# Performance work log

Measured on AMD Instinct MI355X. Metric: run time of the kernel, lower is better.

## Reference

```python
import jax, jax.numpy as jnp
import numpy as np

N_HEADS = 16


def _apply_rope(x, cos, sin):
    # x: (B, T, H, hd); cos/sin: (max_len, hd//2)
    B, T, H, hd = x.shape
    c = cos[:T][None, :, None, :]  # (1, T, 1, hd//2)
    s = sin[:T][None, :, None, :]
    x1 = x[..., 0::2]
    x2 = x[..., 1::2]
    y1 = x1 * c - x2 * s
    y2 = x1 * s + x2 * c
    return jnp.stack((y1, y2), axis=-1).reshape(B, T, H, hd)


def _precompute_rope(head_dim, max_len):
    theta = 10000.0
    inv = 1.0 / theta ** (np.arange(0, head_dim, 2, dtype=np.float32) / head_dim)
    t = np.arange(max_len, dtype=np.float32)
    freqs = np.outer(t, inv)
    return jnp.asarray(np.cos(freqs)), jnp.asarray(np.sin(freqs))


def setup_inputs() -> dict:
    key = jax.random.key(0)
    k1, k2, k3 = jax.random.split(key, 3)
    B, T, C = 4, 2048, 2048
    hd = C // N_HEADS
    x = jax.random.normal(k1, (B, T, C), dtype=jnp.float32)
    w_attn = jax.random.normal(k2, (C, 3 * C), dtype=jnp.float32) * (C ** -0.5)
    w_proj = jax.random.normal(k3, (C, C), dtype=jnp.float32) * (C ** -0.5)
    rope_cos, rope_sin = _precompute_rope(hd, T)
    return {"x": x, "w_attn": w_attn, "w_proj": w_proj,
            "rope_cos": rope_cos, "rope_sin": rope_sin}


def reference(x, w_attn, w_proj, rope_cos, rope_sin):
    B, T, C = x.shape
    H = N_HEADS
    hd = C // H
    qkv = x @ w_attn  # (B, T, 3C)
    q, k, v = jnp.split(qkv, 3, axis=2)
    q = q.reshape(B, T, H, hd)
    k = k.reshape(B, T, H, hd)
    v = v.reshape(B, T, H, hd)
    q = _apply_rope(q, rope_cos, rope_sin)
    k = _apply_rope(k, rope_cos, rope_sin)
    scale = 1.0 / jnp.sqrt(jnp.asarray(hd, dtype=x.dtype))
    scores = jnp.einsum('bqhd,bkhd->bhqk', q, k) * scale  # (B, H, T, T)
    causal = jnp.tril(jnp.ones((T, T), dtype=bool))
    scores = jnp.where(causal[None, None], scores, jnp.finfo(scores.dtype).min)
    attn = jax.nn.softmax(scores, axis=-1)
    y = jnp.einsum('bhqk,bkhd->bqhd', attn, v).reshape(B, T, C)
    return y @ w_proj
```

## Files before the change

### kernel.cpp

```cpp
#include <hip/hip_runtime.h>
#include <cstdint>
#include <cstddef>

#define DEVI __device__ __forceinline__

typedef __attribute__((ext_vector_type(8))) short bf16x8;
typedef __attribute__((ext_vector_type(4))) float f32x4;

DEVI unsigned short f2bf(float f) {
  unsigned int u = __float_as_uint(f);
  u += 0x7fffu + ((u >> 16) & 1u);
  return (unsigned short)(u >> 16);
}
DEVI float bf2f(unsigned int us) { return __uint_as_float(us << 16); }

DEVI void gld_lds16(const void* g, void* l) {
  __builtin_amdgcn_global_load_lds(
      (const __attribute__((address_space(1))) void*)g,
      (__attribute__((address_space(3))) void*)l, 16, 0, 0);
}

__global__ __launch_bounds__(256) void k_conv(const float* __restrict__ in,
                                              short* __restrict__ out, int n4) {
  int i = blockIdx.x * 256 + threadIdx.x;
  if (i >= n4) return;
  float4 v = reinterpret_cast<const float4*>(in)[i];
  uint2 o;
  o.x = (unsigned)f2bf(v.x) | ((unsigned)f2bf(v.y) << 16);
  o.y = (unsigned)f2bf(v.z) | ((unsigned)f2bf(v.w) << 16);
  reinterpret_cast<uint2*>(out)[i] = o;
}

__global__ __launch_bounds__(256) void k_transpose(const float* __restrict__ in,
                                                   short* __restrict__ out,
                                                   int R, int Cc) {
  __shared__ short tile[64][66];
  int tcols = Cc >> 6;
  int tb = blockIdx.x % tcols;
  int rb = blockIdx.x / tcols;
  int tid = threadIdx.x;
#pragma unroll
  for (int rep = 0; rep < 16; ++rep) {
    int idx = rep * 256 + tid;
    int r = idx >> 6, c = idx & 63;
    tile[r][c] = (short)f2bf(in[(size_t)(rb * 64 + r) * Cc + tb * 64 + c]);
  }
  __syncthreads();
#pragma unroll
  for (int rep = 0; rep < 16; ++rep) {
    int idx = rep * 256 + tid;
    int r = idx >> 6, c = idx & 63;
    out[(size_t)(tb * 64 + r) * R + rb * 64 + c] = tile[c][r];
  }
}

template <int MODE, typename OutT>
__global__ __launch_bounds__(512, 2) void k_gemm8(const short* __restrict__ A,
                                                  const short* __restrict__ BT,
                                                  OutT* __restrict__ C,
                                                  int M, int N, int K,
                                                  const float* __restrict__ cosb,
                                                  const float* __restrict__ sinb,
                                                  short* __restrict__ Qr,
                                                  short* __restrict__ Kr,
                                                  short* __restrict__ VT) {
  __shared__ short sA[4][8192];
  __shared__ short sB[4][8192];
  const int tid = threadIdx.x;
  const int wv = tid >> 6, lane = tid & 63;
  const int l16 = lane & 15, lhi = lane >> 4;
  const int wr = wv >> 2, wc = wv & 3;
  const int bm = blockIdx.x * 256, bn = blockIdx.y * 256;
  const int srow0 = wv * 16 + (lane >> 2);
  const int sgs = lane & 3;
  const int NT = K >> 5;

  auto stageA = [&](int kt, int b) {
#pragma unroll
    for (int j = 0; j < 2; ++j) {
      int row = j * 128 + srow0;
      int g = sgs ^ ((row >> 1) & 3);
      gld_lds16(A + (size_t)(bm + row) * K + kt + g * 8,
                &sA[b][j * 4096 + wv * 512]);
    }
  };
  auto stageB = [&](int kt, int b) {
#pragma unroll
    for (int j = 0; j < 2; ++j) {
      int row = j * 128 + srow0;
      int g = sgs ^ ((row >> 1) & 3);
      gld_lds16(BT + (size_t)(bn + row) * K + kt + g * 8,
                &sB[b][j * 4096 + wv * 512]);
    }
  };

  f32x4 acc[8][4] = {};
  bf16x8 aP[8], bP[4], aQ[8], bQ[4];

#define FRAG_READ(DA, DB, BUF)                                                 \
  {                                                                            \
    const short* bufA_ = sA[(BUF)];                                            \
    const short* bufB_ = sB[(BUF)];                                            \
    _Pragma("unroll") for (int n = 0; n < 4; ++n) {                            \
      int row = wc * 64 + n * 16 + l16;                                        \
      DB[n] = *(const bf16x8*)&bufB_[row * 32 + ((lhi ^ ((row >> 1) & 3)) << 3)]; \
    }                                                                          \
    _Pragma("unroll") for (int m = 0; m < 8; ++m) {                            \
      int row = wr * 128 + m * 16 + l16;                                       \
      DA[m] = *(const bf16x8*)&bufA_[row * 32 + ((lhi ^ ((row >> 1) & 3)) << 3)]; \
    }                                                                          \
  }

#define TILE_BODY(T, CA, CB, NA, NB)                                           \
  {                                                                            \
    const int t_ = (T);                                                        \
    if (t_ + 1 < NT) FRAG_READ(NA, NB, (t_ + 1) & 3);                          \
    if (t_ + 3 < NT) {                                                         \
      stageA((t_ + 3) * 32, (t_ + 3) & 3);                                     \
      stageB((t_ + 3) * 32, (t_ + 3) & 3);                                     \
    }                                                                          \
    __builtin_amdgcn_sched_barrier(0);                                         \
    if (t_ + 3 < NT) {                                                         \
      asm volatile("s_waitcnt vmcnt(4)" ::: "memory");                         \
    } else {                                                                   \
      asm volatile("s_waitcnt vmcnt(0)" ::: "memory");                         \
    }                                                                          \
    __builtin_amdgcn_sched_barrier(0);                                         \
    __builtin_amdgcn_s_setprio(1);                                             \
    _Pragma("unroll") for (int m = 0; m < 8; ++m)                              \
        _Pragma("unroll") for (int n = 0; n < 4; ++n)                          \
            acc[m][n] = __builtin_amdgcn_mfma_f32_16x16x32_bf16(               \
                CA[m], CB[n], acc[m][n], 0, 0, 0);                             \
    __builtin_amdgcn_s_setprio(0);                                             \
    __builtin_amdgcn_sched_barrier(0);                                         \
    __builtin_amdgcn_s_barrier();                                              \
    __builtin_amdgcn_sched_barrier(0);                                         \
  }

  stageA(0, 0); stageB(0, 0);
  stageA(32, 1); stageB(32, 1);
  stageA(64, 2); stageB(64, 2);
  asm volatile("s_waitcnt vmcnt(8)" ::: "memory");
  __builtin_amdgcn_s_barrier();
  FRAG_READ(aP, bP, 0);
  asm volatile("s_waitcnt vmcnt(4)" ::: "memory");
  __builtin_amdgcn_s_barrier();
  __builtin_amdgcn_sched_barrier(0);

  for (int t = 0; t < NT; t += 2) {
    TILE_BODY(t, aP, bP, aQ, bQ);
    TILE_BODY(t + 1, aQ, bQ, aP, bP);
  }
#undef FRAG_READ
#undef TILE_BODY

  if constexpr (MODE == 1) {
#pragma unroll
    for (int m = 0; m < 8; ++m) {
#pragma unroll
      for (int n = 0; n < 4; ++n) {
        int col = bn + wc * 64 + n * 16 + l16;
#pragma unroll
        for (int r = 0; r < 4; ++r) {
          int row = bm + wr * 128 + m * 16 + lhi * 4 + r;
          C[(size_t)row * N + col] = acc[m][n][r];
        }
      }
    }
  } else {
    const int part = bn >> 11;
    const float kC = 0.08838834764831845f * 1.44269504088896340f;
    if (part < 2) {
      const float qs = (part == 0) ? kC : 1.0f;
      short* dst = (part == 0) ? Qr : Kr;
#pragma unroll
      for (int m = 0; m < 8; ++m) {
#pragma unroll
        for (int n = 0; n < 4; ++n) {
          int colm = (bn & 2047) + wc * 64 + n * 16 + l16;
          int h = colm >> 7, d = colm & 127;
          int p = d >> 1;
          bool ev = (d & 1) == 0;
#pragma unroll
          for (int r = 0; r < 4; ++r) {
            int row = bm + wr * 128 + m * 16 + lhi * 4 + r;
            int b = row >> 11, t = row & 2047;
            float c = cosb[t * 64 + p];
            float s = sinb[t * 64 + p];
            float x = acc[m][n][r];
            float xp = __shfl_xor(x, 1);
            float y = ev ? (x * c - xp * s) : (xp * s + x * c);
            dst[((size_t)(b * 16 + h) * 2048 + t) * 128 + d] =
                (short)f2bf(y * qs);
          }
        }
      }
    } else {
#pragma unroll
      for (int m = 0; m < 8; ++m) {
#pragma unroll
        for (int n = 0; n < 4; ++n) {
          int colm = (bn & 2047) + wc * 64 + n * 16 + l16;
          int h = colm >> 7, d = colm & 127;
#pragma unroll
          for (int r = 0; r < 4; ++r) {
            int row = bm + wr * 128 + m * 16 + lhi * 4 + r;
            int b = row >> 11, t = row & 2047;
            VT[((size_t)(b * 16 + h) * 128 + d) * 2048 + t] =
                (short)f2bf(acc[m][n][r]);
          }
        }
      }
    }
  }
}

__global__ __launch_bounds__(256) void k_attn(const short* __restrict__ Qr,
                                              const short* __restrict__ Kr,
                                              const short* __restrict__ VT,
                                              short* __restrict__ Y) {
  __shared__ short sK[2][64 * 128];
  __shared__ short sVT[2][128 * 64];
  __shared__ short sP[4][16 * 64];
  const int tid = threadIdx.x, wv = tid >> 6, lane = tid & 63;
  const int l8r = lane >> 3, l8c = lane & 7, l16 = lane & 15, lhi = lane >> 4;
  const int bid = blockIdx.x;
  const int pair = bid & 15, bh = bid >> 4;
  const size_t base = (size_t)bh * 2048 * 128;
  const int b = bh >> 4, h = bh & 15;

  const short ob = (short)0x3F80;
  const bf16x8 ones = {ob, ob, ob, ob, ob, ob, ob, ob};

  auto stage = [&](int kv0, int buf) {
#pragma unroll
    for (int rr = 0; rr < 4; ++rr) {
      int ch = rr * 4 + wv;
      {
        int row = ch * 4 + lhi;
        int wch = l16 ^ (row & 7);
        gld_lds16(Kr + base + (size_t)(kv0 + row) * 128 + wch * 8,
                  &sK[buf][ch * 512]);
      }
      {
        int drow = ch * 8 + l8r;
        int wch = l8c ^ (drow & 7);
        gld_lds16(VT + base + (size_t)drow * 2048 + kv0 + wch * 8,
                  &sVT[buf][ch * 512]);
      }
    }
  };

  for (int half = 0; half < 2; ++half) {
    const int qt = half ? 31 - pair : pair;
    const int q0 = qt * 64;
    const int nt = qt + 1;

    bf16x8 qf[4];
    const int qrow = q0 + wv * 16 + l16;
#pragma unroll
    for (int ks = 0; ks < 4; ++ks)
      qf[ks] = *reinterpret_cast<const bf16x8*>(Qr + base + (size_t)qrow * 128 +
                                                ks * 32 + lhi * 8);

    f32x4 acc_o[8] = {};
    f32x4 acc_l = {};
    float m_run[4];
#pragma unroll
    for (int r = 0; r < 4; ++r) m_run[r] = -1e30f;

    stage(0, 0);
    __syncthreads();

    for (int it = 0; it < nt; ++it) {
      const int cur = it & 1;
      if (it + 1 < nt) stage((it + 1) * 64, cur ^ 1);

      f32x4 sacc[4] = {};
#pragma unroll
      for (int cf = 0; cf < 4; ++cf) {
        int krow = cf * 16 + l16;
#pragma unroll
        for (int ks = 0; ks < 4; ++ks) {
          int e = krow * 128 + ks * 32 + lhi * 8;
          bf16x8 kf = *reinterpret_cast<const bf16x8*>(
              &sK[cur][e ^ ((krow & 7) << 3)]);
          sacc[cf] = __builtin_amdgcn_mfma_f32_16x16x32_bf16(qf[ks], kf,
                                                             sacc[cf], 0, 0, 0);
        }
      }

      if (it == nt - 1) {
#pragma unroll
        for (int cf = 0; cf < 4; ++cf) {
          int col = cf * 16 + l16;
#pragma unroll
          for (int r = 0; r < 4; ++r)
            if (col > wv * 16 + lhi * 4 + r) sacc[cf][r] = -3e38f;
        }
      }

      bool exceed = false;
#pragma unroll
      for (int cf = 0; cf < 4; ++cf)
#pragma unroll
        for (int r = 0; r < 4; ++r)
          exceed |= (sacc[cf][r] > m_run[r] + 8.f);

      if (__any(exceed)) {
        float resc[4];
#pragma unroll
        for (int r = 0; r < 4; ++r) {
          float mx = fmaxf(fmaxf(sacc[0][r], sacc[1][r]),
                           fmaxf(sacc[2][r], sacc[3][r]));
          mx = fmaxf(mx, __shfl_xor(mx, 1));
          mx = fmaxf(mx, __shfl_xor(mx, 2));
          mx = fmaxf(mx, __shfl_xor(mx, 4));
          mx = fmaxf(mx, __shfl_xor(mx, 8));
          float mnew = fmaxf(m_run[r], mx);
          resc[r] = exp2f(m_run[r] - mnew);
          m_run[r] = mnew;
        }
#pragma unroll
        for (int df = 0; df < 8; ++df)
#pragma unroll
          for (int r = 0; r < 4; ++r) acc_o[df][r] *= resc[r];
#pragma unroll
        for (int r = 0; r < 4; ++r) acc_l[r] *= resc[r];
      }

#pragma unroll
      for (int cf = 0; cf < 4; ++cf)
#pragma unroll
        for (int r = 0; r < 4; ++r) {
          float p = exp2f(sacc[cf][r] - m_run[r]);
          int prow = lhi * 4 + r;
          int e = prow * 64 + cf * 16 + l16;
          sP[wv][e ^ ((prow & 7) << 3)] = (short)f2bf(p);
        }

#pragma unroll
      for (int kk = 0; kk < 2; ++kk) {
        int e = l16 * 64 + kk * 32 + lhi * 8;
        bf16x8 pa = *reinterpret_cast<const bf16x8*>(
            &sP[wv][e ^ ((l16 & 7) << 3)]);
        acc_l = __builtin_amdgcn_mfma_f32_16x16x32_bf16(pa, ones, acc_l, 0, 0, 0);
#pragma unroll
        for (int df = 0; df < 8; ++df) {
          int vrow = df * 16 + l16;
          int ev = vrow * 64 + kk * 32 + lhi * 8;
          bf16x8 vb = *reinterpret_cast<const bf16x8*>(
              &sVT[cur][ev ^ ((vrow & 7) << 3)]);
          acc_o[df] = __builtin_amdgcn_mfma_f32_16x16x32_bf16(pa, vb,
                                                              acc_o[df], 0, 0, 0);
        }
      }
      __syncthreads();
    }

    float inv[4];
#pragma unroll
    for (int r = 0; r < 4; ++r) inv[r] = 1.f / acc_l[r];
#pragma unroll
    for (int df = 0; df < 8; ++df) {
      int col = h * 128 + df * 16 + l16;
#pragma unroll
      for (int r = 0; r < 4; ++r) {
        int row = q0 + wv * 16 + lhi * 4 + r;
        Y[((size_t)b * 2048 + row) * 2048 + col] =
            (short)f2bf(acc_o[df][r] * inv[r]);
      }
    }
  }
}

extern "C" void kernel_launch(void* const* d_in, const int* in_sizes, int n_in,
                              void* d_out, int out_size, void* d_ws, size_t ws_size,
                              hipStream_t stream) {
  const float* x        = (const float*)d_in[0];
  const float* w_attn   = (const float*)d_in[1];
  const float* w_proj   = (const float*)d_in[2];
  const float* rope_cos = (const float*)d_in[3];
  const float* rope_sin = (const float*)d_in[4];

  char* ws = (char*)d_ws;
  short* xbf    = (short*)(ws);
  short* wattnT = (short*)(ws + 33554432ull);
  short* wprojT = (short*)(ws + 58720256ull);
  short* Y      = (short*)(ws + 67108864ull);
  short* Qr     = (short*)(ws + 167772160ull);
  short* Kr     = (short*)(ws + 201326592ull);
  short* VT     = (short*)(ws + 234881024ull);

  k_conv<<<16384, 256, 0, stream>>>(x, xbf, 4194304);
  k_transpose<<<3072, 256, 0, stream>>>(w_attn, wattnT, 2048, 6144);
  k_transpose<<<1024, 256, 0, stream>>>(w_proj, wprojT, 2048, 2048);
  k_gemm8<2, short><<<dim3(32, 24), 512, 0, stream>>>(
      xbf, wattnT, (short*)nullptr, 8192, 6144, 2048,
      rope_cos, rope_sin, Qr, Kr, VT);
  k_attn<<<1024, 256, 0, stream>>>(Qr, Kr, VT, Y);
  k_gemm8<1, float><<<dim3(32, 8), 512, 0, stream>>>(
      Y, wprojT, (float*)d_out, 8192, 2048, 2048,
      nullptr, nullptr, nullptr, nullptr, nullptr);
}
```

Baseline: 473.1 us.

## Shrink GEMM tiles to 128x128 with 256-thread blocks and simpler pipeline

The bf16 GEMM kernel moves from 256x256 tiles with 8 waves to 128x128 tiles with 4 waves and 4 blocks per CU. It also drops the explicit register double-buffering of fragments for a simpler loop that reads fragments from LDS and runs MFMAs within each iteration. The goal is more blocks per CU, so latency is hidden by occupancy rather than manual software pipelining. In exchange, per-tile data reuse is lower, global and LDS traffic per FLOP rises, and LDS reads are no longer overlapped with the MFMAs.

```diff
diff --git a/kernel.cpp b/kernel.cpp
--- a/kernel.cpp
+++ b/kernel.cpp
@@ -55,7 +55,7 @@
 }
 
 template <int MODE, typename OutT>
-__global__ __launch_bounds__(512, 2) void k_gemm8(const short* __restrict__ A,
+__global__ __launch_bounds__(256, 4) void k_gemm8(const short* __restrict__ A,
                                                   const short* __restrict__ BT,
                                                   OutT* __restrict__ C,
                                                   int M, int N, int K,
@@ -64,105 +64,85 @@
                                                   short* __restrict__ Qr,
                                                   short* __restrict__ Kr,
                                                   short* __restrict__ VT) {
-  __shared__ short sA[4][8192];
-  __shared__ short sB[4][8192];
+  __shared__ short sA[4][4096];
+  __shared__ short sB[4][4096];
   const int tid = threadIdx.x;
   const int wv = tid >> 6, lane = tid & 63;
   const int l16 = lane & 15, lhi = lane >> 4;
-  const int wr = wv >> 2, wc = wv & 3;
-  const int bm = blockIdx.x * 256, bn = blockIdx.y * 256;
-  const int srow0 = wv * 16 + (lane >> 2);
-  const int sgs = lane & 3;
+  const int wr = wv >> 1, wc = wv & 1;
+  const int bm = blockIdx.x * 128, bn = blockIdx.y * 128;
   const int NT = K >> 5;
 
-  auto stageA = [&](int kt, int b) {
+  auto stage = [&](int kt, int b) {
 #pragma unroll
     for (int j = 0; j < 2; ++j) {
-      int row = j * 128 + srow0;
-      int g = sgs ^ ((row >> 1) & 3);
+      int slot = j * 256 + tid;
+      int row = slot >> 2;
+      int g = (slot & 3) ^ ((row >> 1) & 3);
       gld_lds16(A + (size_t)(bm + row) * K + kt + g * 8,
-                &sA[b][j * 4096 + wv * 512]);
+                &sA[b][j * 2048 + wv * 512]);
+    }
+#pragma unroll
+    for (int j = 0; j < 2; ++j) {
+      int slot = j * 256 + tid;
+      int row = slot >> 2;
+      int g = (slot & 3) ^ ((row >> 1) & 3);
+      gld_lds16(BT + (size_t)(bn + row) * K + kt + g * 8,
+                &sB[b][j * 2048 + wv * 512]);
     }
   };
-  auto stageB = [&](int kt, int b) {
-#pragma unroll
-    for (int j = 0; j < 2; ++j) {
-      int row = j * 128 + srow0;
-      int g = sgs ^ ((row >> 1) & 3);
-      gld_lds16(BT + (size_t)(bn + row) * K + kt + g * 8,
-                &sB[b][j * 4096 + wv * 512]);
-    }
-  };
-
-  f32x4 acc[8][4] = {};
-  bf16x8 aP[8], bP[4], aQ[8], bQ[4];
-
-#define FRAG_READ(DA, DB, BUF)                                                 \
-  {                                                                            \
-    const short* bufA_ = sA[(BUF)];                                            \
-    const short* bufB_ = sB[(BUF)];                                            \
-    _Pragma("unroll") for (int n = 0; n < 4; ++n) {                            \
-      int row = wc * 64 + n * 16 + l16;                                        \
-      DB[n] = *(const bf16x8*)&bufB_[row * 32 + ((lhi ^ ((row >> 1) & 3)) << 3)]; \
-    }                                                                          \
-    _Pragma("unroll") for (int m = 0; m < 8; ++m) {                            \
-      int row = wr * 128 + m * 16 + l16;                                       \
-      DA[m] = *(const bf16x8*)&bufA_[row * 32 + ((lhi ^ ((row >> 1) & 3)) << 3)]; \
-    }                                                                          \
-  }
-
-#define TILE_BODY(T, CA, CB, NA, NB)                                           \
-  {                                                                            \
-    const int t_ = (T);                                                        \
-    if (t_ + 1 < NT) FRAG_READ(NA, NB, (t_ + 1) & 3);                          \
-    if (t_ + 3 < NT) {                                                         \
-      stageA((t_ + 3) * 32, (t_ + 3) & 3);                                     \
-      stageB((t_ + 3) * 32, (t_ + 3) & 3);                                     \
-    }                                                                          \
-    __builtin_amdgcn_sched_barrier(0);                                         \
-    if (t_ + 3 < NT) {                                                         \
-      asm volatile("s_waitcnt vmcnt(4)" ::: "memory");                         \
-    } else {                                                                   \
-      asm volatile("s_waitcnt vmcnt(0)" ::: "memory");                         \
-    }                                                                          \
-    __builtin_amdgcn_sched_barrier(0);                                         \
-    __builtin_amdgcn_s_setprio(1);                                             \
-    _Pragma("unroll") for (int m = 0; m < 8; ++m)                              \
-        _Pragma("unroll") for (int n = 0; n < 4; ++n)                          \
-            acc[m][n] = __builtin_amdgcn_mfma_f32_16x16x32_bf16(               \
-                CA[m], CB[n], acc[m][n], 0, 0, 0);                             \
-    __builtin_amdgcn_s_setprio(0);                                             \
-    __builtin_amdgcn_sched_barrier(0);                                         \
-    __builtin_amdgcn_s_barrier();                                              \
-    __builtin_amdgcn_sched_barrier(0);                                         \
-  }
-
-  stageA(0, 0); stageB(0, 0);
-  stageA(32, 1); stageB(32, 1);
-  stageA(64, 2); stageB(64, 2);
+
+  f32x4 acc[4][4] = {};
+
+  stage(0, 0);
+  stage(32, 1);
+  stage(64, 2);
   asm volatile("s_waitcnt vmcnt(8)" ::: "memory");
   __builtin_amdgcn_s_barrier();
-  FRAG_READ(aP, bP, 0);
-  asm volatile("s_waitcnt vmcnt(4)" ::: "memory");
-  __builtin_amdgcn_s_barrier();
-  __builtin_amdgcn_sched_barrier(0);
-
-  for (int t = 0; t < NT; t += 2) {
-    TILE_BODY(t, aP, bP, aQ, bQ);
-    TILE_BODY(t + 1, aQ, bQ, aP, bP);
-  }
-#undef FRAG_READ
-#undef TILE_BODY
+
+  for (int t = 0; t < NT; ++t) {
+    const int cur = t & 3;
+    if (t + 3 < NT) stage((t + 3) * 32, (t + 3) & 3);
+    bf16x8 af[4], bf[4];
+    const short* bufA = sA[cur];
+    const short* bufB = sB[cur];
+#pragma unroll
+    for (int m = 0; m < 4; ++m) {
+      int row = wr * 64 + m * 16 + l16;
+      af[m] = *(const bf16x8*)&bufA[row * 32 + ((lhi ^ ((row >> 1) & 3)) << 3)];
+    }
+#pragma unroll
+    for (int n = 0; n < 4; ++n) {
+      int row = wc * 64 + n * 16 + l16;
+      bf[n] = *(const bf16x8*)&bufB[row * 32 + ((lhi ^ ((row >> 1) & 3)) << 3)];
+    }
+    __builtin_amdgcn_s_setprio(1);
+#pragma unroll
+    for (int m = 0; m < 4; ++m)
+#pragma unroll
+      for (int n = 0; n < 4; ++n)
+        acc[m][n] = __builtin_amdgcn_mfma_f32_16x16x32_bf16(af[m], bf[n],
+                                                            acc[m][n], 0, 0, 0);
+    __builtin_amdgcn_s_setprio(0);
+    if (t + 3 < NT) {
+      asm volatile("s_waitcnt vmcnt(8)" ::: "memory");
+    } else if (t + 2 < NT) {
+      asm volatile("s_waitcnt vmcnt(4)" ::: "memory");
+    } else if (t + 1 < NT) {
+      asm volatile("s_waitcnt vmcnt(0)" ::: "memory");
+    }
+    __builtin_amdgcn_s_barrier();
+  }
 
   if constexpr (MODE == 1) {
 #pragma unroll
-    for (int m = 0; m < 8; ++m) {
+    for (int m = 0; m < 4; ++m) {
 #pragma unroll
       for (int n = 0; n < 4; ++n) {
         int col = bn + wc * 64 + n * 16 + l16;
 #pragma unroll
         for (int r = 0; r < 4; ++r) {
-          int row = bm + wr * 128 + m * 16 + lhi * 4 + r;
+          int row = bm + wr * 64 + m * 16 + lhi * 4 + r;
           C[(size_t)row * N + col] = acc[m][n][r];
         }
       }
@@ -174,7 +154,7 @@
       const float qs = (part == 0) ? kC : 1.0f;
       short* dst = (part == 0) ? Qr : Kr;
 #pragma unroll
-      for (int m = 0; m < 8; ++m) {
+      for (int m = 0; m < 4; ++m) {
 #pragma unroll
         for (int n = 0; n < 4; ++n) {
           int colm = (bn & 2047) + wc * 64 + n * 16 + l16;
@@ -183,7 +163,7 @@
           bool ev = (d & 1) == 0;
 #pragma unroll
           for (int r = 0; r < 4; ++r) {
-            int row = bm + wr * 128 + m * 16 + lhi * 4 + r;
+            int row = bm + wr * 64 + m * 16 + lhi * 4 + r;
             int b = row >> 11, t = row & 2047;
             float c = cosb[t * 64 + p];
             float s = sinb[t * 64 + p];
@@ -197,14 +177,14 @@
       }
     } else {
 #pragma unroll
-      for (int m = 0; m < 8; ++m) {
+      for (int m = 0; m < 4; ++m) {
 #pragma unroll
         for (int n = 0; n < 4; ++n) {
           int colm = (bn & 2047) + wc * 64 + n * 16 + l16;
           int h = colm >> 7, d = colm & 127;
 #pragma unroll
           for (int r = 0; r < 4; ++r) {
-            int row = bm + wr * 128 + m * 16 + lhi * 4 + r;
+            int row = bm + wr * 64 + m * 16 + lhi * 4 + r;
             int b = row >> 11, t = row & 2047;
             VT[((size_t)(b * 16 + h) * 128 + d) * 2048 + t] =
                 (short)f2bf(acc[m][n][r]);
@@ -395,11 +375,11 @@
   k_conv<<<16384, 256, 0, stream>>>(x, xbf, 4194304);
   k_transpose<<<3072, 256, 0, stream>>>(w_attn, wattnT, 2048, 6144);
   k_transpose<<<1024, 256, 0, stream>>>(w_proj, wprojT, 2048, 2048);
-  k_gemm8<2, short><<<dim3(32, 24), 512, 0, stream>>>(
+  k_gemm8<2, short><<<dim3(64, 48), 256, 0, stream>>>(
       xbf, wattnT, (short*)nullptr, 8192, 6144, 2048,
       rope_cos, rope_sin, Qr, Kr, VT);
   k_attn<<<1024, 256, 0, stream>>>(Qr, Kr, VT, Y);
-  k_gemm8<1, float><<<dim3(32, 8), 512, 0, stream>>>(
+  k_gemm8<1, float><<<dim3(64, 16), 256, 0, stream>>>(
       Y, wprojT, (float*)d_out, 8192, 2048, 2048,
       nullptr, nullptr, nullptr, nullptr, nullptr);
 }
```

Result: slower. 592.9 us (+25.3%).

## Prefetch K/V through registers into a single LDS buffer with MFMA priority

Applied to the files above, without the earlier changes.

The attention kernel drops the double-buffered direct global-to-LDS loads. It now prefetches the next K and V^T tile into registers during compute, then writes them into a single swizzled LDS buffer after a barrier. This halves the K/V shared memory footprint, which may allow more resident blocks per CU, and s_setprio raises wave priority around the MFMA loops. The cost is extra VGPRs for the staging registers, an additional __syncthreads per iteration, and LDS stores on the critical path.

```diff
diff --git a/kernel.cpp b/kernel.cpp
--- a/kernel.cpp
+++ b/kernel.cpp
@@ -179,14 +179,14 @@
         for (int n = 0; n < 4; ++n) {
           int colm = (bn & 2047) + wc * 64 + n * 16 + l16;
           int h = colm >> 7, d = colm & 127;
-          int p = d >> 1;
+          int p2 = d >> 1;
           bool ev = (d & 1) == 0;
 #pragma unroll
           for (int r = 0; r < 4; ++r) {
             int row = bm + wr * 128 + m * 16 + lhi * 4 + r;
             int b = row >> 11, t = row & 2047;
-            float c = cosb[t * 64 + p];
-            float s = sinb[t * 64 + p];
+            float c = cosb[t * 64 + p2];
+            float s = sinb[t * 64 + p2];
             float x = acc[m][n][r];
             float xp = __shfl_xor(x, 1);
             float y = ev ? (x * c - xp * s) : (xp * s + x * c);
@@ -219,11 +219,11 @@
                                               const short* __restrict__ Kr,
                                               const short* __restrict__ VT,
                                               short* __restrict__ Y) {
-  __shared__ short sK[2][64 * 128];
-  __shared__ short sVT[2][128 * 64];
+  __shared__ short sK[64 * 128];
+  __shared__ short sVT[128 * 64];
   __shared__ short sP[4][16 * 64];
   const int tid = threadIdx.x, wv = tid >> 6, lane = tid & 63;
-  const int l8r = lane >> 3, l8c = lane & 7, l16 = lane & 15, lhi = lane >> 4;
+  const int l16 = lane & 15, lhi = lane >> 4;
   const int bid = blockIdx.x;
   const int pair = bid & 15, bh = bid >> 4;
   const size_t base = (size_t)bh * 2048 * 128;
@@ -232,22 +232,39 @@
   const short ob = (short)0x3F80;
   const bf16x8 ones = {ob, ob, ob, ob, ob, ob, ob, ob};
 
-  auto stage = [&](int kv0, int buf) {
-#pragma unroll
-    for (int rr = 0; rr < 4; ++rr) {
-      int ch = rr * 4 + wv;
-      {
-        int row = ch * 4 + lhi;
-        int wch = l16 ^ (row & 7);
-        gld_lds16(Kr + base + (size_t)(kv0 + row) * 128 + wch * 8,
-                  &sK[buf][ch * 512]);
-      }
-      {
-        int drow = ch * 8 + l8r;
-        int wch = l8c ^ (drow & 7);
-        gld_lds16(VT + base + (size_t)drow * 2048 + kv0 + wch * 8,
-                  &sVT[buf][ch * 512]);
-      }
+  uint4 kreg[4], vreg[4];
+  auto loadKV = [&](int kv0) {
+#pragma unroll
+    for (int j = 0; j < 4; ++j) {
+      int slot = j * 256 + tid;
+      int row = slot >> 4, c16 = slot & 15;
+      kreg[j] = *reinterpret_cast<const uint4*>(
+          Kr + base + (size_t)(kv0 + row) * 128 + c16 * 8);
+    }
+#pragma unroll
+    for (int j = 0; j < 4; ++j) {
+      int slot = j * 256 + tid;
+      int row = slot >> 3, g = slot & 7;
+      vreg[j] = *reinterpret_cast<const uint4*>(
+          VT + base + (size_t)row * 2048 + kv0 + g * 8);
+    }
+  };
+  auto writeKV = [&]() {
+#pragma unroll
+    for (int j = 0; j < 4; ++j) {
+      int slot = j * 256 + tid;
+      int row = slot >> 4, c16 = slot & 15;
+      *reinterpret_cast<uint4*>(
+          reinterpret_cast<char*>(sK) + row * 256 + ((c16 ^ (row & 7)) << 4)) =
+          kreg[j];
+    }
+#pragma unroll
+    for (int j = 0; j < 4; ++j) {
+      int slot = j * 256 + tid;
+      int row = slot >> 3, g = slot & 7;
+      *reinterpret_cast<uint4*>(
+          reinterpret_cast<char*>(sVT) + row * 128 + ((g ^ (row & 7)) << 4)) =
+          vreg[j];
     }
   };
 
@@ -269,14 +286,17 @@
 #pragma unroll
     for (int r = 0; r < 4; ++r) m_run[r] = -1e30f;
 
-    stage(0, 0);
+    loadKV(0);
+    writeKV();
     __syncthreads();
 
     for (int it = 0; it < nt; ++it) {
-      const int cur = it & 1;
-      if (it + 1 < nt) stage((it + 1) * 64, cur ^ 1);
+      const bool pf = (it + 1 < nt);
+      if (pf) loadKV((it + 1) * 64);
+      __builtin_amdgcn_sched_barrier(0);
 
       f32x4 sacc[4] = {};
+      __builtin_amdgcn_s_setprio(1);
 #pragma unroll
       for (int cf = 0; cf < 4; ++cf) {
         int krow = cf * 16 + l16;
@@ -284,11 +304,12 @@
         for (int ks = 0; ks < 4; ++ks) {
           int e = krow * 128 + ks * 32 + lhi * 8;
           bf16x8 kf = *reinterpret_cast<const bf16x8*>(
-              &sK[cur][e ^ ((krow & 7) << 3)]);
+              &sK[e ^ ((krow & 7) << 3)]);
           sacc[cf] = __builtin_amdgcn_mfma_f32_16x16x32_bf16(qf[ks], kf,
                                                              sacc[cf], 0, 0, 0);
         }
       }
+      __builtin_amdgcn_s_setprio(0);
 
       if (it == nt - 1) {
 #pragma unroll
@@ -339,6 +360,7 @@
           sP[wv][e ^ ((prow & 7) << 3)] = (short)f2bf(p);
         }
 
+      __builtin_amdgcn_s_setprio(1);
 #pragma unroll
       for (int kk = 0; kk < 2; ++kk) {
         int e = l16 * 64 + kk * 32 + lhi * 8;
@@ -350,12 +372,18 @@
           int vrow = df * 16 + l16;
           int ev = vrow * 64 + kk * 32 + lhi * 8;
           bf16x8 vb = *reinterpret_cast<const bf16x8*>(
-              &sVT[cur][ev ^ ((vrow & 7) << 3)]);
+              &sVT[ev ^ ((vrow & 7) << 3)]);
           acc_o[df] = __builtin_amdgcn_mfma_f32_16x16x32_bf16(pa, vb,
                                                               acc_o[df], 0, 0, 0);
         }
       }
+      __builtin_amdgcn_s_setprio(0);
+
       __syncthreads();
+      if (pf) {
+        writeKV();
+        __syncthreads();
+      }
     }
 
     float inv[4];
```

After: 654.3 us. 38.3% more time.

## Halve attention KV tile to 32 with new LDS swizzle and MFMA priority hints

Applied to the files above, without the earlier changes.

Shrinks the flash-attention KV tile from 64 to 32 keys, halving LDS use for the K, V^T and P buffers, and doubles the iteration count. It adds a new XOR swizzle for the 32-wide V^T and P layouts and extends causal masking to the last two tiles. It also wraps the MFMA sections in s_setprio hints. The smaller LDS footprint may allow more resident blocks per CU and gives finer causal granularity, at the cost of twice as many barriers and softmax rescale checks per query tile.

```diff
diff --git a/kernel.cpp b/kernel.cpp
--- a/kernel.cpp
+++ b/kernel.cpp
@@ -179,14 +179,14 @@
         for (int n = 0; n < 4; ++n) {
           int colm = (bn & 2047) + wc * 64 + n * 16 + l16;
           int h = colm >> 7, d = colm & 127;
-          int p = d >> 1;
+          int p2 = d >> 1;
           bool ev = (d & 1) == 0;
 #pragma unroll
           for (int r = 0; r < 4; ++r) {
             int row = bm + wr * 128 + m * 16 + lhi * 4 + r;
             int b = row >> 11, t = row & 2047;
-            float c = cosb[t * 64 + p];
-            float s = sinb[t * 64 + p];
+            float c = cosb[t * 64 + p2];
+            float s = sinb[t * 64 + p2];
             float x = acc[m][n][r];
             float xp = __shfl_xor(x, 1);
             float y = ev ? (x * c - xp * s) : (xp * s + x * c);
@@ -219,11 +219,11 @@
                                               const short* __restrict__ Kr,
                                               const short* __restrict__ VT,
                                               short* __restrict__ Y) {
-  __shared__ short sK[2][64 * 128];
-  __shared__ short sVT[2][128 * 64];
-  __shared__ short sP[4][16 * 64];
+  __shared__ short sK[2][32 * 128];
+  __shared__ short sVT[2][128 * 32];
+  __shared__ short sP[4][16 * 32];
   const int tid = threadIdx.x, wv = tid >> 6, lane = tid & 63;
-  const int l8r = lane >> 3, l8c = lane & 7, l16 = lane & 15, lhi = lane >> 4;
+  const int l16 = lane & 15, lhi = lane >> 4;
   const int bid = blockIdx.x;
   const int pair = bid & 15, bh = bid >> 4;
   const size_t base = (size_t)bh * 2048 * 128;
@@ -234,18 +234,18 @@
 
   auto stage = [&](int kv0, int buf) {
 #pragma unroll
-    for (int rr = 0; rr < 4; ++rr) {
+    for (int rr = 0; rr < 2; ++rr) {
       int ch = rr * 4 + wv;
       {
         int row = ch * 4 + lhi;
-        int wch = l16 ^ (row & 7);
-        gld_lds16(Kr + base + (size_t)(kv0 + row) * 128 + wch * 8,
+        int g = l16 ^ (row & 7);
+        gld_lds16(Kr + base + (size_t)(kv0 + row) * 128 + g * 8,
                   &sK[buf][ch * 512]);
       }
       {
-        int drow = ch * 8 + l8r;
-        int wch = l8c ^ (drow & 7);
-        gld_lds16(VT + base + (size_t)drow * 2048 + kv0 + wch * 8,
+        int drow = ch * 16 + (lane >> 2);
+        int g = (lane & 3) ^ ((drow >> 1) & 3);
+        gld_lds16(VT + base + (size_t)drow * 2048 + kv0 + g * 8,
                   &sVT[buf][ch * 512]);
       }
     }
@@ -254,7 +254,7 @@
   for (int half = 0; half < 2; ++half) {
     const int qt = half ? 31 - pair : pair;
     const int q0 = qt * 64;
-    const int nt = qt + 1;
+    const int nt = 2 * qt + 2;
 
     bf16x8 qf[4];
     const int qrow = q0 + wv * 16 + l16;
@@ -274,26 +274,28 @@
 
     for (int it = 0; it < nt; ++it) {
       const int cur = it & 1;
-      if (it + 1 < nt) stage((it + 1) * 64, cur ^ 1);
-
-      f32x4 sacc[4] = {};
-#pragma unroll
-      for (int cf = 0; cf < 4; ++cf) {
+      if (it + 1 < nt) stage((it + 1) * 32, cur ^ 1);
+
+      f32x4 sacc[2] = {};
+      __builtin_amdgcn_s_setprio(1);
+#pragma unroll
+      for (int cf = 0; cf < 2; ++cf) {
         int krow = cf * 16 + l16;
 #pragma unroll
         for (int ks = 0; ks < 4; ++ks) {
-          int e = krow * 128 + ks * 32 + lhi * 8;
-          bf16x8 kf = *reinterpret_cast<const bf16x8*>(
-              &sK[cur][e ^ ((krow & 7) << 3)]);
+          int e = krow * 128 + (((ks * 4 + lhi) ^ (krow & 7)) << 3);
+          bf16x8 kf = *reinterpret_cast<const bf16x8*>(&sK[cur][e]);
           sacc[cf] = __builtin_amdgcn_mfma_f32_16x16x32_bf16(qf[ks], kf,
                                                              sacc[cf], 0, 0, 0);
         }
       }
-
-      if (it == nt - 1) {
-#pragma unroll
-        for (int cf = 0; cf < 4; ++cf) {
-          int col = cf * 16 + l16;
+      __builtin_amdgcn_s_setprio(0);
+
+      if (it >= nt - 2) {
+        const int rel = it * 32 - q0;
+#pragma unroll
+        for (int cf = 0; cf < 2; ++cf) {
+          int col = rel + cf * 16 + l16;
 #pragma unroll
           for (int r = 0; r < 4; ++r)
             if (col > wv * 16 + lhi * 4 + r) sacc[cf][r] = -3e38f;
@@ -302,7 +304,7 @@
 
       bool exceed = false;
 #pragma unroll
-      for (int cf = 0; cf < 4; ++cf)
+      for (int cf = 0; cf < 2; ++cf)
 #pragma unroll
         for (int r = 0; r < 4; ++r)
           exceed |= (sacc[cf][r] > m_run[r] + 8.f);
@@ -311,8 +313,7 @@
         float resc[4];
 #pragma unroll
         for (int r = 0; r < 4; ++r) {
-          float mx = fmaxf(fmaxf(sacc[0][r], sacc[1][r]),
-                           fmaxf(sacc[2][r], sacc[3][r]));
+          float mx = fmaxf(sacc[0][r], sacc[1][r]);
           mx = fmaxf(mx, __shfl_xor(mx, 1));
           mx = fmaxf(mx, __shfl_xor(mx, 2));
           mx = fmaxf(mx, __shfl_xor(mx, 4));
@@ -330,31 +331,31 @@
       }
 
 #pragma unroll
-      for (int cf = 0; cf < 4; ++cf)
+      for (int cf = 0; cf < 2; ++cf)
 #pragma unroll
         for (int r = 0; r < 4; ++r) {
           float p = exp2f(sacc[cf][r] - m_run[r]);
           int prow = lhi * 4 + r;
-          int e = prow * 64 + cf * 16 + l16;
-          sP[wv][e ^ ((prow & 7) << 3)] = (short)f2bf(p);
-        }
-
-#pragma unroll
-      for (int kk = 0; kk < 2; ++kk) {
-        int e = l16 * 64 + kk * 32 + lhi * 8;
-        bf16x8 pa = *reinterpret_cast<const bf16x8*>(
-            &sP[wv][e ^ ((l16 & 7) << 3)]);
+          int c = cf * 16 + l16;
+          int s = prow * 32 + ((((c >> 3) ^ ((prow >> 1) & 3)) << 3)) + (c & 7);
+          sP[wv][s] = (short)f2bf(p);
+        }
+
+      __builtin_amdgcn_s_setprio(1);
+      {
+        int e = l16 * 32 + ((lhi ^ ((l16 >> 1) & 3)) << 3);
+        bf16x8 pa = *reinterpret_cast<const bf16x8*>(&sP[wv][e]);
         acc_l = __builtin_amdgcn_mfma_f32_16x16x32_bf16(pa, ones, acc_l, 0, 0, 0);
 #pragma unroll
         for (int df = 0; df < 8; ++df) {
           int vrow = df * 16 + l16;
-          int ev = vrow * 64 + kk * 32 + lhi * 8;
-          bf16x8 vb = *reinterpret_cast<const bf16x8*>(
-              &sVT[cur][ev ^ ((vrow & 7) << 3)]);
+          int ev = vrow * 32 + ((lhi ^ ((vrow >> 1) & 3)) << 3);
+          bf16x8 vb = *reinterpret_cast<const bf16x8*>(&sVT[cur][ev]);
           acc_o[df] = __builtin_amdgcn_mfma_f32_16x16x32_bf16(pa, vb,
                                                               acc_o[df], 0, 0, 0);
         }
       }
+      __builtin_amdgcn_s_setprio(0);
       __syncthreads();
     }
 
```

Measured after the change: 491.0 us. +3.8%, slower.
